# Kernel tuning notes

Hardware: AMD Instinct MI355X
Metric: run time of the kernel (lower is better)

The kernel has to match this reference:

```python
import jax, jax.numpy as jnp
import numpy as np

T = 5
EPS = 1e-05


def setup_inputs() -> dict:
    key = jax.random.key(0)
    X = jax.random.normal(key, (64, 512, 32, 32), dtype=jnp.float32)
    return {"X": X}


def reference(X):
    # IterNorm (training branch): whiten channels via Newton-Schulz inverse sqrt.
    N, C, H, W = X.shape
    x = jnp.transpose(X, (1, 0, 2, 3)).reshape(C, -1)  # [d, m], d=C, m=N*H*W
    d, m = x.shape
    mean = jnp.mean(x, axis=-1, keepdims=True)
    xc = x - mean
    I = jnp.eye(d, dtype=X.dtype)
    # Sigma = eps*I + (1/m) xc xc^T  (addmm(eps, I, 1/m, xc, xc^T))
    Sigma = EPS * I + (xc @ xc.T) / m
    rTr = 1.0 / jnp.trace(Sigma)          # (Sigma * I).sum().reciprocal()
    Sigma_N = Sigma * rTr
    P = I
    for _ in range(T):
        # P_{k+1} = 1.5*P_k - 0.5 * P_k^3 @ Sigma_N
        P = 1.5 * P - 0.5 * (P @ P @ P) @ Sigma_N
    wm = P * jnp.sqrt(rTr)                # whitening matrix ~ Sigma^{-1/2}
    xn = wm @ xc                          # [d, m]
    Xn = jnp.transpose(xn.reshape(C, N, H, W), (1, 0, 2, 3))
    return Xn
```

## Files before the change

kernel.cpp:

```cpp
#include <hip/hip_runtime.h>
#include <math.h>

#define Nn   64
#define Cc   512
#define HWs  1024
#define CHW  (Cc * HWs)
#define Mm   (Nn * HWs)
#define EPSC 1e-5f
#define NBC  128

typedef unsigned int   u32;
typedef unsigned short u16;
typedef __attribute__((ext_vector_type(8))) short  short8;
typedef __attribute__((ext_vector_type(4))) float  floatx4;

__device__ __forceinline__ u16 f2bf(float f) {
    u32 u = __float_as_uint(f);
    u += 0x7fff + ((u >> 16) & 1);
    return (u16)(u >> 16);
}
__device__ __forceinline__ float bf2f(u16 h) {
    return __uint_as_float(((u32)h) << 16);
}

__device__ __forceinline__ void gld_lds16(const u16* g, u16* l) {
    __builtin_amdgcn_global_load_lds(
        (const __attribute__((address_space(1))) u32*)g,
        (__attribute__((address_space(3))) u32*)l, 16, 0, 0);
}

__global__ __launch_bounds__(256) void convert_transpose(const float* __restrict__ X,
                                                         u16* __restrict__ Xbf,
                                                         u16* __restrict__ Xt,
                                                         float* __restrict__ meanP) {
    const int hT = blockIdx.x;
    const int h0 = hT << 6;
    const int c0 = blockIdx.y << 6;
    const int n  = blockIdx.z;
    const int t  = threadIdx.x;
    __shared__ u16   T[64][65];
    __shared__ float red[64][17];

    const float* Xn  = X   + (size_t)n * CHW;
    u16*         Xbn = Xbf + (size_t)n * CHW;
    u16*         Xtn = Xt  + (size_t)n * CHW;

    const int cl = t >> 4;
    const int h4 = (t & 15) << 2;
#pragma unroll
    for (int i = 0; i < 4; ++i) {
        const int c = cl + (i << 4);
        float4 v = *(const float4*)&Xn[(size_t)(c0 + c) * HWs + h0 + h4];
        red[c][t & 15] = v.x + v.y + v.z + v.w;
        u16 b0 = f2bf(v.x), b1 = f2bf(v.y), b2 = f2bf(v.z), b3 = f2bf(v.w);
        *(ushort4*)&Xbn[(size_t)(c0 + c) * HWs + h0 + h4] = make_ushort4(b0, b1, b2, b3);
        T[c][h4]     = b0;
        T[c][h4 + 1] = b1;
        T[c][h4 + 2] = b2;
        T[c][h4 + 3] = b3;
    }
    __syncthreads();
    const int hl = t >> 4;
    const int c4 = (t & 15) << 2;
#pragma unroll
    for (int i = 0; i < 4; ++i) {
        const int h = hl + (i << 4);
        ushort4 pk = make_ushort4(T[c4][h], T[c4 + 1][h], T[c4 + 2][h], T[c4 + 3][h]);
        *(ushort4*)&Xtn[(size_t)(h0 + h) * Cc + c0 + c4] = pk;
    }
    if (t < 64) {
        float s = 0.f;
#pragma unroll
        for (int j = 0; j < 16; ++j) s += red[t][j];
        atomicAdd(&meanP[hT * 512 + c0 + t], s);
    }
}

__global__ __launch_bounds__(256) void gram_mfma(const u16* __restrict__ Xbf,
                                                 float* __restrict__ G) {
    static const int TI[10] = {0,0,0,0,1,1,1,2,2,3};
    static const int TJ[10] = {0,1,2,3,1,2,3,2,3,3};
    const int id = blockIdx.x;
    const int q  = id >> 3;
    const int x  = q % 10;
    const int y  = (id & 7) + ((q / 10) << 3);
    const int i0 = TI[x] << 7;
    const int j0 = TJ[x] << 7;
    const int n0 = y << 1;
    const int t  = threadIdx.x;
    const int w  = t >> 6, l = t & 63;

    __shared__ u16 As[128 * 32];
    __shared__ u16 Bs[128 * 32];

    floatx4 acc[4][4];
#pragma unroll
    for (int mi = 0; mi < 4; ++mi)
#pragma unroll
        for (int ni = 0; ni < 4; ++ni) acc[mi][ni] = (floatx4){0.f, 0.f, 0.f, 0.f};

    const int lr = l >> 2;
    const int lc = (l & 3) << 3;
    const int wm = w >> 1, wn = w & 1;
    const int fm = l & 15, fq = l >> 4;

    for (int n = n0; n < n0 + 2; ++n) {
        const u16* Xn = Xbf + (size_t)n * CHW;
        for (int hw = 0; hw < HWs; hw += 32) {
#pragma unroll
            for (int p = 0; p < 2; ++p) {
                const int g   = w * 2 + p;
                const int row = g * 16 + lr;
                gld_lds16(Xn + (size_t)(i0 + row) * HWs + hw + lc, &As[g * 512]);
                gld_lds16(Xn + (size_t)(j0 + row) * HWs + hw + lc, &Bs[g * 512]);
            }
            __syncthreads();
            short8 a[4], b[4];
#pragma unroll
            for (int mi = 0; mi < 4; ++mi)
                a[mi] = *(const short8*)&As[(wm * 64 + mi * 16 + fm) * 32 + fq * 8];
#pragma unroll
            for (int ni = 0; ni < 4; ++ni)
                b[ni] = *(const short8*)&Bs[(wn * 64 + ni * 16 + fm) * 32 + fq * 8];
#pragma unroll
            for (int mi = 0; mi < 4; ++mi)
#pragma unroll
                for (int ni = 0; ni < 4; ++ni)
                    acc[mi][ni] = __builtin_amdgcn_mfma_f32_16x16x32_bf16(
                        a[mi], b[ni], acc[mi][ni], 0, 0, 0);
            __syncthreads();
        }
    }
#pragma unroll
    for (int mi = 0; mi < 4; ++mi)
#pragma unroll
        for (int ni = 0; ni < 4; ++ni)
#pragma unroll
            for (int r = 0; r < 4; ++r) {
                const int gi = i0 + wm * 64 + mi * 16 + fq * 4 + r;
                const int gj = j0 + wn * 64 + ni * 16 + fm;
                atomicAdd(&G[(size_t)gi * Cc + gj], acc[mi][ni][r]);
            }
}

__device__ __forceinline__ void gridbar(int* bar, int gen) {
    __syncthreads();
    if (threadIdx.x == 0) {
        __threadfence();
        __hip_atomic_fetch_add(bar, 1, __ATOMIC_RELAXED, __HIP_MEMORY_SCOPE_AGENT);
        while (__hip_atomic_load(bar, __ATOMIC_RELAXED, __HIP_MEMORY_SCOPE_AGENT) < gen * NBC)
            __builtin_amdgcn_s_sleep(1);
        __threadfence();
    }
    __syncthreads();
}

__device__ __forceinline__ void mm_panel(const u16* Ah, const u16* Al,
                                         const u16* Bh, const u16* Bl,
                                         int i0, int j0,
                                         float alpha, const float* D, float beta,
                                         float* Cf, u16* Ch, u16* Cl, u16* S) {
    const int t = threadIdx.x, w = t >> 6, l = t & 63;
    const int wm = w >> 1, wn = w & 1, fm = l & 15, fq = l >> 4;
    const u16* src = (w == 0) ? Ah : (w == 1) ? Al : (w == 2) ? Bh : Bl;
    const int rbase = (w < 2) ? i0 : j0;
    const int lr = l >> 2, lc = (l & 3) << 3;

    floatx4 acc[2][2];
#pragma unroll
    for (int mi = 0; mi < 2; ++mi)
#pragma unroll
        for (int ni = 0; ni < 2; ++ni) acc[mi][ni] = (floatx4){0.f, 0.f, 0.f, 0.f};

    auto issue = [&](int cc, int bb) {
        u16* dst = S + bb * 32768 + w * 8192;
        const u16* sp = src + (size_t)rbase * 512 + cc * 128;
#pragma unroll
        for (int s = 0; s < 4; ++s)
#pragma unroll
            for (int g = 0; g < 4; ++g)
                gld_lds16(sp + (size_t)(g * 16 + lr) * 512 + s * 32 + lc,
                          dst + s * 2048 + g * 512);
    };
    auto compute = [&](int bb) {
        const u16* base = S + bb * 32768;
#pragma unroll
        for (int s = 0; s < 4; ++s) {
            short8 ah[2], al[2], bh[2], bl[2];
#pragma unroll
            for (int mi = 0; mi < 2; ++mi) {
                const int ro = s * 2048 + (wm * 32 + mi * 16 + fm) * 32 + fq * 8;
                ah[mi] = *(const short8*)&base[ro];
                al[mi] = *(const short8*)&base[8192 + ro];
            }
#pragma unroll
            for (int ni = 0; ni < 2; ++ni) {
                const int ro = s * 2048 + (wn * 32 + ni * 16 + fm) * 32 + fq * 8;
                bh[ni] = *(const short8*)&base[16384 + ro];
                bl[ni] = *(const short8*)&base[24576 + ro];
            }
#pragma unroll
            for (int mi = 0; mi < 2; ++mi)
#pragma unroll
                for (int ni = 0; ni < 2; ++ni) {
                    acc[mi][ni] = __builtin_amdgcn_mfma_f32_16x16x32_bf16(ah[mi], bh[ni], acc[mi][ni], 0, 0, 0);
                    acc[mi][ni] = __builtin_amdgcn_mfma_f32_16x16x32_bf16(ah[mi], bl[ni], acc[mi][ni], 0, 0, 0);
                    acc[mi][ni] = __builtin_amdgcn_mfma_f32_16x16x32_bf16(al[mi], bh[ni], acc[mi][ni], 0, 0, 0);
                }
        }
    };

    issue(0, 0); issue(1, 1);
    __syncthreads();
    compute(0);
    compute(1);
    __syncthreads();
    issue(2, 0); issue(3, 1);
    __syncthreads();
    compute(0);
    compute(1);

#pragma unroll
    for (int mi = 0; mi < 2; ++mi)
#pragma unroll
        for (int ni = 0; ni < 2; ++ni)
#pragma unroll
            for (int r4 = 0; r4 < 4; ++r4) {
                const int gi = i0 + wm * 32 + mi * 16 + fq * 4 + r4;
                const int gj = j0 + wn * 32 + ni * 16 + fm;
                const size_t idx = (size_t)gi * 512 + gj;
                float v = alpha * acc[mi][ni][r4];
                if (D) v += beta * D[idx];
                if (Cf) Cf[idx] = v;
                const u16 h = f2bf(v);
                Ch[idx] = h;
                Cl[idx] = f2bf(v - bf2f(h));
            }
}

__global__ __launch_bounds__(256) void ns_chain(
    const float* G, const float* meanP, float* scal, int* bar, float* wmmv,
    u16* Sh, u16* Sl, u16* PhA, u16* PlA, u16* PhB, u16* PlB,
    u16* T2h, u16* T2l, u16* Wh, u16* Wl, float* PfA, float* PfB) {
    __shared__ u16   S[65536];
    __shared__ float meanL[512];
    __shared__ float redL[4];
    const int t = threadIdx.x, b = blockIdx.x;
    const int w = t >> 6, l = t & 63;

    float tp = 0.f;
#pragma unroll
    for (int cb = 0; cb < 2; ++cb) {
        const int c = t + (cb << 8);
        float s = 0.f;
#pragma unroll
        for (int q = 0; q < 16; ++q) s += meanP[(q << 9) + c];
        const float mc = s * (1.0f / Mm);
        meanL[c] = mc;
        tp += G[(size_t)c * 513] * (1.0f / Mm) - mc * mc;
    }
#pragma unroll
    for (int o = 32; o > 0; o >>= 1) tp += __shfl_xor(tp, o);
    if (l == 0) redL[w] = tp;
    __syncthreads();
    const float tr  = redL[0] + redL[1] + redL[2] + redL[3] + (float)Cc * EPSC;
    const float rtr = 1.0f / tr;
    const float sr  = sqrtf(rtr);
    if (b == 0 && t == 0) { scal[0] = rtr; scal[1] = sr; }

#pragma unroll
    for (int k2 = 0; k2 < 8; ++k2) {
        const int e = (b << 11) + (k2 << 8) + t;
        const int i = e >> 9, j = e & 511;
        const float g = (i <= j) ? G[((size_t)i << 9) + j] : G[((size_t)j << 9) + i];
        float sig = g * (1.0f / Mm) - meanL[i] * meanL[j];
        if (i == j) sig += EPSC;
        const float sN = sig * rtr;
        const u16 sh = f2bf(sN);
        Sh[e] = sh;
        Sl[e] = f2bf(sN - bf2f(sh));
        const float p1 = ((i == j) ? 1.5f : 0.f) - 0.5f * sN;
        PfA[e] = p1;
        const u16 ph = f2bf(p1);
        PhA[e] = ph;
        PlA[e] = f2bf(p1 - bf2f(ph));
    }
    int gen = 0;
    gridbar(bar, ++gen);

    u16 *ph = PhA, *pl = PlA, *qh = PhB, *ql = PlB;
    float *pf = PfA, *qf = PfB;
    const int i0 = ((b & 63) >> 3) << 6, j0 = (b & 7) << 6;
    for (int it = 0; it < 4; ++it) {
        if (b < 64)
            mm_panel(ph, pl, ph, pl, i0, j0, 1.f, nullptr, 0.f,
                     nullptr, T2h, T2l, S);
        else
            mm_panel(ph, pl, Sh, Sl, i0, j0, 1.f, nullptr, 0.f,
                     nullptr, Wh, Wl, S);
        gridbar(bar, ++gen);
        if (b < 64)
            mm_panel(T2h, T2l, Wh, Wl, i0, j0, -0.5f, pf, 1.5f,
                     qf, qh, ql, S);
        gridbar(bar, ++gen);
        { u16* x = ph; ph = qh; qh = x; }
        { u16* x = pl; pl = ql; ql = x; }
        { float* x = pf; pf = qf; qf = x; }
    }

    {
        const int c = (b << 2) + (t >> 6);
        float s = 0.f;
#pragma unroll
        for (int jj = 0; jj < 8; ++jj) {
            const int j = l + (jj << 6);
            s += pf[((size_t)c << 9) + j] * meanL[j];
        }
#pragma unroll
        for (int o = 32; o > 0; o >>= 1) s += __shfl_xor(s, o);
        if (l == 0) wmmv[c] = s * sr;
    }
}

__global__ __launch_bounds__(256) void whiten_mfma(const u16* __restrict__ Xt,
                                                   const u16* __restrict__ Pbf,
                                                   const float* __restrict__ wmm,
                                                   const float* __restrict__ scal,
                                                   float* __restrict__ out) {
    const int id  = blockIdx.x;
    const int m   = (id >> 3) & 3;
    const int grp = (id & 7) + ((id >> 5) << 3);
    const int c0  = m << 7;
    const int h0  = (grp & 7) << 7;
    const int n   = grp >> 3;
    const int t   = threadIdx.x;
    const int w   = t >> 6, l = t & 63;

    __shared__ char smem[128 * 68 * 4];
    u16* As = (u16*)smem;
    u16* Bs = As + 4096;
    float* Ep = (float*)smem;

    floatx4 acc[4][4];
#pragma unroll
    for (int mi = 0; mi < 4; ++mi)
#pragma unroll
        for (int ni = 0; ni < 4; ++ni) acc[mi][ni] = (floatx4){0.f, 0.f, 0.f, 0.f};

    const int lr = l >> 2;
    const int lc = (l & 3) << 3;
    const int wm = w >> 1, wn = w & 1;
    const int fm = l & 15, fq = l >> 4;

    const u16* Xn = Xt + (size_t)n * CHW;

    for (int kk = 0; kk < Cc; kk += 32) {
#pragma unroll
        for (int p = 0; p < 2; ++p) {
            const int g   = w * 2 + p;
            const int row = g * 16 + lr;
            gld_lds16(Xn  + (size_t)(h0 + row) * Cc + kk + lc, &As[g * 512]);
            gld_lds16(Pbf + (size_t)(c0 + row) * Cc + kk + lc, &Bs[g * 512]);
        }
        __syncthreads();
        short8 a[4], b[4];
#pragma unroll
        for (int mi = 0; mi < 4; ++mi)
            a[mi] = *(const short8*)&As[(wm * 64 + mi * 16 + fm) * 32 + fq * 8];
#pragma unroll
        for (int ni = 0; ni < 4; ++ni)
            b[ni] = *(const short8*)&Bs[(wn * 64 + ni * 16 + fm) * 32 + fq * 8];
#pragma unroll
        for (int mi = 0; mi < 4; ++mi)
#pragma unroll
            for (int ni = 0; ni < 4; ++ni)
                acc[mi][ni] = __builtin_amdgcn_mfma_f32_16x16x32_bf16(
                    a[mi], b[ni], acc[mi][ni], 0, 0, 0);
        __syncthreads();
    }

    const float sr = scal[1];
    float wv[4];
#pragma unroll
    for (int ni = 0; ni < 4; ++ni) wv[ni] = wmm[c0 + wn * 64 + ni * 16 + fm];
    float* outn = out + (size_t)n * CHW;

#pragma unroll
    for (int mp = 0; mp < 2; ++mp) {
        __syncthreads();
#pragma unroll
        for (int p = 0; p < 2; ++p) {
            const int mi = mp * 2 + p;
#pragma unroll
            for (int ni = 0; ni < 4; ++ni) {
                const int row  = wn * 64 + ni * 16 + fm;
                const int slot = wm * 32 + p * 16 + fq * 4;
                floatx4 v = acc[mi][ni] * sr - wv[ni];
                *(floatx4*)&Ep[row * 68 + slot] = v;
            }
        }
        __syncthreads();
#pragma unroll
        for (int jj = 0; jj < 8; ++jj) {
            const int idx = jj * 256 + t;
            const int row = idx >> 4;
            const int s4  = (idx & 15) << 2;
            const int wmr = s4 >> 5;
            const int within = s4 & 31;
            float4 v = *(const float4*)&Ep[row * 68 + s4];
            *(float4*)&outn[(size_t)(c0 + row) * HWs + h0 + wmr * 64 + mp * 32 + within] = v;
        }
    }
}

__global__ __launch_bounds__(256) void mean_kernel(const float* __restrict__ X,
                                                   float* __restrict__ mean) {
    const int c = blockIdx.x;
    const int t = threadIdx.x;
    float s = 0.f;
    for (int n = 0; n < Nn; ++n) {
        const float4* p = (const float4*)(X + (size_t)n * CHW + (size_t)c * HWs);
        float4 v = p[t];
        s += v.x + v.y + v.z + v.w;
    }
    __shared__ float red[256];
    red[t] = s;
    __syncthreads();
    for (int o = 128; o > 0; o >>= 1) {
        if (t < o) red[t] += red[t + o];
        __syncthreads();
    }
    if (t == 0) mean[c] = red[0] * (1.0f / Mm);
}

__global__ __launch_bounds__(256) void trace_fb(const float* __restrict__ G,
                                                const float* __restrict__ mean,
                                                float* __restrict__ scal) {
    const int t = threadIdx.x;
    float s = 0.f;
    for (int i = t; i < Cc; i += 256)
        s += G[(size_t)i * Cc + i] * (1.0f / Mm) - mean[i] * mean[i];
    __shared__ float red[256];
    red[t] = s;
    __syncthreads();
    for (int o = 128; o > 0; o >>= 1) {
        if (t < o) red[t] += red[t + o];
        __syncthreads();
    }
    if (t == 0) {
        const float tr  = red[0] + (float)Cc * EPSC;
        const float rtr = 1.0f / tr;
        scal[0] = rtr;
        scal[1] = sqrtf(rtr);
    }
}

__global__ __launch_bounds__(256) void gram_kernel(const float* __restrict__ X,
                                                   float* __restrict__ G) {
    const int ti = blockIdx.x >> 3, tj = blockIdx.x & 7;
    const int i0 = ti << 6, j0 = tj << 6;
    const int n0 = blockIdx.y << 3;
    const int t  = threadIdx.x;
    const int tx = t & 15, ty = t >> 4;
    __shared__ float As[64][33];
    __shared__ float Bs[64][33];
    float acc[4][4] = {};
    const int lc = t & 31;
    const int lr0 = t >> 5;
    for (int n = n0; n < n0 + 8; ++n) {
        const float* Xn = X + (size_t)n * CHW;
        for (int hw0 = 0; hw0 < HWs; hw0 += 32) {
#pragma unroll
            for (int r = 0; r < 8; ++r) {
                const int row = lr0 + (r << 3);
                As[row][lc] = Xn[(size_t)(i0 + row) * HWs + hw0 + lc];
                Bs[row][lc] = Xn[(size_t)(j0 + row) * HWs + hw0 + lc];
            }
            __syncthreads();
#pragma unroll
            for (int k = 0; k < 32; ++k) {
                float a[4], b[4];
#pragma unroll
                for (int r = 0; r < 4; ++r) a[r] = As[(ty << 2) + r][k];
#pragma unroll
                for (int cn = 0; cn < 4; ++cn) b[cn] = Bs[(tx << 2) + cn][k];
#pragma unroll
                for (int r = 0; r < 4; ++r)
#pragma unroll
                    for (int cn = 0; cn < 4; ++cn) acc[r][cn] += a[r] * b[cn];
            }
            __syncthreads();
        }
    }
#pragma unroll
    for (int r = 0; r < 4; ++r)
#pragma unroll
        for (int cn = 0; cn < 4; ++cn)
            atomicAdd(&G[(size_t)(i0 + (ty << 2) + r) * Cc + j0 + (tx << 2) + cn],
                      acc[r][cn]);
}

__global__ __launch_bounds__(256) void sigman_full_kernel(const float* __restrict__ G,
                                                          const float* __restrict__ mean,
                                                          const float* __restrict__ scal,
                                                          float* __restrict__ S,
                                                          float* __restrict__ P) {
    const int e = blockIdx.x * 256 + threadIdx.x;
    const int i = e >> 9, j = e & 511;
    const float rtr = scal[0];
    float sig = G[e] * (1.0f / Mm) - mean[i] * mean[j];
    if (i == j) sig += EPSC;
    S[e] = sig * rtr;
    P[e] = (i == j) ? 1.f : 0.f;
}

__global__ __launch_bounds__(256) void mm512_kernel(const float* __restrict__ A,
                                                    const float* __restrict__ B,
                                                    float* __restrict__ C,
                                                    float alpha,
                                                    const float* __restrict__ D,
                                                    float beta) {
    const int ti = blockIdx.x >> 3, tj = blockIdx.x & 7;
    const int i0 = ti << 6, j0 = tj << 6;
    const int t  = threadIdx.x;
    const int tx = t & 15, ty = t >> 4;
    __shared__ float As[64][33];
    __shared__ float Bs[32][65];
    float acc[4][4] = {};
    const int lcA = t & 31, lrA = t >> 5;
    const int lcB = t & 63, lrB = t >> 6;
    for (int k0 = 0; k0 < 512; k0 += 32) {
#pragma unroll
        for (int r = 0; r < 8; ++r) {
            const int row = lrA + (r << 3);
            As[row][lcA] = A[(size_t)(i0 + row) * 512 + k0 + lcA];
        }
#pragma unroll
        for (int r = 0; r < 8; ++r) {
            const int row = lrB + (r << 2);
            Bs[row][lcB] = B[(size_t)(k0 + row) * 512 + j0 + lcB];
        }
        __syncthreads();
#pragma unroll
        for (int k = 0; k < 32; ++k) {
            float a[4], b[4];
#pragma unroll
            for (int r = 0; r < 4; ++r) a[r] = As[(ty << 2) + r][k];
#pragma unroll
            for (int cn = 0; cn < 4; ++cn) b[cn] = Bs[k][(tx << 2) + cn];
#pragma unroll
            for (int r = 0; r < 4; ++r)
#pragma unroll
                for (int cn = 0; cn < 4; ++cn) acc[r][cn] += a[r] * b[cn];
        }
        __syncthreads();
    }
#pragma unroll
    for (int r = 0; r < 4; ++r) {
        const size_t idx = (size_t)(i0 + (ty << 2) + r) * 512 + j0 + (tx << 2);
        float4 v;
        v.x = alpha * acc[r][0];
        v.y = alpha * acc[r][1];
        v.z = alpha * acc[r][2];
        v.w = alpha * acc[r][3];
        if (D) {
            const float4 d = *(const float4*)(D + idx);
            v.x += beta * d.x; v.y += beta * d.y; v.z += beta * d.z; v.w += beta * d.w;
        }
        *(float4*)(C + idx) = v;
    }
}

__global__ __launch_bounds__(128) void wmm_kernel(const float* __restrict__ P,
                                                  const float* __restrict__ mean,
                                                  const float* __restrict__ scal,
                                                  float* __restrict__ wmm) {
    const int c = blockIdx.x, t = threadIdx.x;
    float s = 0.f;
    for (int j = t; j < Cc; j += 128) s += P[(size_t)c * Cc + j] * mean[j];
    __shared__ float red[128];
    red[t] = s;
    __syncthreads();
    for (int o = 64; o > 0; o >>= 1) {
        if (t < o) red[t] += red[t + o];
        __syncthreads();
    }
    if (t == 0) wmm[c] = red[0] * scal[1];
}

__global__ __launch_bounds__(256) void whiten_kernel(const float* __restrict__ X,
                                                     const float* __restrict__ P,
                                                     const float* __restrict__ wmm,
                                                     const float* __restrict__ scal,
                                                     float* __restrict__ out) {
    const int c0 = blockIdx.x << 6;
    const int h0 = blockIdx.y << 6;
    const int n  = blockIdx.z;
    const int t  = threadIdx.x;
    const int tx = t & 15, ty = t >> 4;
    __shared__ float Ps[64][33];
    __shared__ float Xs[32][65];
    float acc[4][4] = {};
    const int lcA = t & 31, lrA = t >> 5;
    const int lcB = t & 63, lrB = t >> 6;
    const float* Xn = X + (size_t)n * CHW;
    for (int k0 = 0; k0 < 512; k0 += 32) {
#pragma unroll
        for (int r = 0; r < 8; ++r) {
            const int row = lrA + (r << 3);
            Ps[row][lcA] = P[(size_t)(c0 + row) * 512 + k0 + lcA];
        }
#pragma unroll
        for (int r = 0; r < 8; ++r) {
            const int row = lrB + (r << 2);
            Xs[row][lcB] = Xn[(size_t)(k0 + row) * HWs + h0 + lcB];
        }
        __syncthreads();
#pragma unroll
        for (int k = 0; k < 32; ++k) {
            float a[4], b[4];
#pragma unroll
            for (int r = 0; r < 4; ++r) a[r] = Ps[(ty << 2) + r][k];
#pragma unroll
            for (int cn = 0; cn < 4; ++cn) b[cn] = Xs[k][(tx << 2) + cn];
#pragma unroll
            for (int r = 0; r < 4; ++r)
#pragma unroll
                for (int cn = 0; cn < 4; ++cn) acc[r][cn] += a[r] * b[cn];
        }
        __syncthreads();
    }
    const float sr = scal[1];
#pragma unroll
    for (int r = 0; r < 4; ++r) {
        const int c = c0 + (ty << 2) + r;
        const float wv = wmm[c];
        float4 v;
        v.x = sr * acc[r][0] - wv;
        v.y = sr * acc[r][1] - wv;
        v.z = sr * acc[r][2] - wv;
        v.w = sr * acc[r][3] - wv;
        *(float4*)(out + (size_t)n * CHW + (size_t)c * HWs + h0 + (tx << 2)) = v;
    }
}

extern "C" void kernel_launch(void* const* d_in, const int* in_sizes, int n_in,
                              void* d_out, int out_size, void* d_ws, size_t ws_size,
                              hipStream_t stream) {
    const float* X = (const float*)d_in[0];
    float* out     = (float*)d_out;

    const size_t NU16 = 33554432;
    const size_t NM   = 262144;
    const size_t NEED = NU16 * 2 * 2
                      + NM * 10 * 2
                      + (NM + 8192 + 32 + 512 + 512 + 2 * NM) * 4;

    if (ws_size >= NEED) {
        u16* Xbf = (u16*)d_ws;
        u16* Xt  = Xbf + NU16;
        u16* Sh  = Xt  + NU16;
        u16* Sl  = Sh + NM;
        u16* PhA = Sl + NM;
        u16* PlA = PhA + NM;
        u16* PhB = PlA + NM;
        u16* PlB = PhB + NM;
        u16* T2h = PlB + NM;
        u16* T2l = T2h + NM;
        u16* Wh  = T2l + NM;
        u16* Wl  = Wh + NM;
        float* G     = (float*)(Wl + NM);
        float* meanP = G + NM;
        float* scal  = meanP + 8192;
        int*   bar   = (int*)(scal + 16);
        float* mean  = (float*)(bar + 16);
        float* wmm   = mean + 512;
        float* PfA   = wmm + 512;
        float* PfB   = PfA + NM;

        hipMemsetAsync(G, 0, (NM + 8192 + 32) * sizeof(float), stream);
        convert_transpose<<<dim3(16, 8, 64), 256, 0, stream>>>(X, Xbf, Xt, meanP);
        gram_mfma<<<320, 256, 0, stream>>>(Xbf, G);
        ns_chain<<<NBC, 256, 0, stream>>>(G, meanP, scal, bar, wmm,
                                          Sh, Sl, PhA, PlA, PhB, PlB,
                                          T2h, T2l, Wh, Wl, PfA, PfB);
        whiten_mfma<<<2048, 256, 0, stream>>>(Xt, PhA, wmm, scal, out);
    } else {
        float* ws   = (float*)d_ws;
        float* mean = ws;
        float* wmm  = ws + 512;
        float* scal = ws + 1024;
        float* G    = ws + 2048;
        float* S    = G + 262144;
        float* Pa   = S + 262144;
        float* Pb   = Pa + 262144;
        float* P2   = Pb + 262144;
        float* P3   = P2 + 262144;

        mean_kernel<<<512, 256, 0, stream>>>(X, mean);
        hipMemsetAsync(G, 0, sizeof(float) * 262144, stream);
        gram_kernel<<<dim3(64, 8), 256, 0, stream>>>(X, G);
        trace_fb<<<1, 256, 0, stream>>>(G, mean, scal);
        sigman_full_kernel<<<1024, 256, 0, stream>>>(G, mean, scal, S, Pa);

        float* P  = Pa;
        float* Pn = Pb;
        for (int it = 0; it < 5; ++it) {
            mm512_kernel<<<64, 256, 0, stream>>>(P, P, P2, 1.f, nullptr, 0.f);
            mm512_kernel<<<64, 256, 0, stream>>>(P2, P, P3, 1.f, nullptr, 0.f);
            mm512_kernel<<<64, 256, 0, stream>>>(P3, S, Pn, -0.5f, P, 1.5f);
            float* tmp = P; P = Pn; Pn = tmp;
        }

        wmm_kernel<<<512, 128, 0, stream>>>(P, mean, scal, wmm);
        whiten_kernel<<<dim3(8, 16, 64), 256, 0, stream>>>(X, P, wmm, scal, out);
    }
}
```

Measured before the change: 512.5 us.

## Double-buffer LDS in gram, NS chain and whiten GEMMs; widen gram grid

Adds ping-pong LDS buffers to the gram, whiten and Newton-Schulz panel GEMMs so the next K-slice global-to-LDS load overlaps the current MFMA work. The gram kernel now gives each block one sample instead of two and launches twice as many blocks. The NS chain panel kernel moves from K=128 chunks to K=64 chunks in an 8-step pipelined loop, which halves its LDS footprint. It also uses half-height 32-row tiles so all 128 blocks take part in the second GEMM of each iteration instead of only 64. In exchange there are twice as many atomics into G from the gram kernel and more barriers per tile.

Result: slower. 524.0 us (+2.2%).

```diff
diff --git a/kernel.cpp b/kernel.cpp
--- a/kernel.cpp
+++ b/kernel.cpp
@@ -86,12 +86,12 @@
     const int y  = (id & 7) + ((q / 10) << 3);
     const int i0 = TI[x] << 7;
     const int j0 = TJ[x] << 7;
-    const int n0 = y << 1;
+    const int n  = y;
     const int t  = threadIdx.x;
     const int w  = t >> 6, l = t & 63;
 
-    __shared__ u16 As[128 * 32];
-    __shared__ u16 Bs[128 * 32];
+    __shared__ u16 As[2][4096];
+    __shared__ u16 Bs[2][4096];
 
     floatx4 acc[4][4];
 #pragma unroll
@@ -104,32 +104,37 @@
     const int wm = w >> 1, wn = w & 1;
     const int fm = l & 15, fq = l >> 4;
 
-    for (int n = n0; n < n0 + 2; ++n) {
-        const u16* Xn = Xbf + (size_t)n * CHW;
-        for (int hw = 0; hw < HWs; hw += 32) {
-#pragma unroll
-            for (int p = 0; p < 2; ++p) {
-                const int g   = w * 2 + p;
-                const int row = g * 16 + lr;
-                gld_lds16(Xn + (size_t)(i0 + row) * HWs + hw + lc, &As[g * 512]);
-                gld_lds16(Xn + (size_t)(j0 + row) * HWs + hw + lc, &Bs[g * 512]);
-            }
-            __syncthreads();
-            short8 a[4], b[4];
-#pragma unroll
-            for (int mi = 0; mi < 4; ++mi)
-                a[mi] = *(const short8*)&As[(wm * 64 + mi * 16 + fm) * 32 + fq * 8];
+    const u16* Xn = Xbf + (size_t)n * CHW;
+
+    auto issue = [&](int k, int bb) {
+#pragma unroll
+        for (int p = 0; p < 2; ++p) {
+            const int g   = w * 2 + p;
+            const int row = g * 16 + lr;
+            gld_lds16(Xn + (size_t)(i0 + row) * HWs + (k << 5) + lc, &As[bb][g * 512]);
+            gld_lds16(Xn + (size_t)(j0 + row) * HWs + (k << 5) + lc, &Bs[bb][g * 512]);
+        }
+    };
+
+    issue(0, 0);
+    __syncthreads();
+    for (int k = 0; k < 32; ++k) {
+        if (k < 31) issue(k + 1, (k + 1) & 1);
+        const int bb = k & 1;
+        short8 a[4], b[4];
+#pragma unroll
+        for (int mi = 0; mi < 4; ++mi)
+            a[mi] = *(const short8*)&As[bb][(wm * 64 + mi * 16 + fm) * 32 + fq * 8];
+#pragma unroll
+        for (int ni = 0; ni < 4; ++ni)
+            b[ni] = *(const short8*)&Bs[bb][(wn * 64 + ni * 16 + fm) * 32 + fq * 8];
+#pragma unroll
+        for (int mi = 0; mi < 4; ++mi)
 #pragma unroll
             for (int ni = 0; ni < 4; ++ni)
-                b[ni] = *(const short8*)&Bs[(wn * 64 + ni * 16 + fm) * 32 + fq * 8];
-#pragma unroll
-            for (int mi = 0; mi < 4; ++mi)
-#pragma unroll
-                for (int ni = 0; ni < 4; ++ni)
-                    acc[mi][ni] = __builtin_amdgcn_mfma_f32_16x16x32_bf16(
-                        a[mi], b[ni], acc[mi][ni], 0, 0, 0);
-            __syncthreads();
-        }
+                acc[mi][ni] = __builtin_amdgcn_mfma_f32_16x16x32_bf16(
+                    a[mi], b[ni], acc[mi][ni], 0, 0, 0);
+        __syncthreads();
     }
 #pragma unroll
     for (int mi = 0; mi < 4; ++mi)
@@ -155,52 +160,63 @@
     __syncthreads();
 }
 
-__device__ __forceinline__ void mm_panel(const u16* Ah, const u16* Al,
-                                         const u16* Bh, const u16* Bl,
-                                         int i0, int j0,
-                                         float alpha, const float* D, float beta,
-                                         float* Cf, u16* Ch, u16* Cl, u16* S) {
+template <int MR>
+__device__ __forceinline__ void mm_bk64(const u16* Ah, const u16* Al,
+                                        const u16* Bh, const u16* Bl,
+                                        int i0, int j0,
+                                        float alpha, const float* D, float beta,
+                                        float* Cf, u16* Ch, u16* Cl, u16* S) {
     const int t = threadIdx.x, w = t >> 6, l = t & 63;
     const int wm = w >> 1, wn = w & 1, fm = l & 15, fq = l >> 4;
-    const u16* src = (w == 0) ? Ah : (w == 1) ? Al : (w == 2) ? Bh : Bl;
+    const int lr = l >> 2, lc = (l & 3) << 3;
+    constexpr int MI     = MR / 32;
+    constexpr int OFF_AL = MR * 64;
+    constexpr int OFF_BH = 2 * MR * 64;
+    constexpr int OFF_BL = 2 * MR * 64 + 4096;
+    constexpr int BUFSZ  = 2 * MR * 64 + 8192;
+
+    const u16* src  = (w == 0) ? Ah : (w == 1) ? Al : (w == 2) ? Bh : Bl;
     const int rbase = (w < 2) ? i0 : j0;
-    const int lr = l >> 2, lc = (l & 3) << 3;
-
-    floatx4 acc[2][2];
-#pragma unroll
-    for (int mi = 0; mi < 2; ++mi)
+    const int R     = (w < 2) ? MR : 64;
+    const int OFF   = (w == 0) ? 0 : (w == 1) ? OFF_AL : (w == 2) ? OFF_BH : OFF_BL;
+
+    floatx4 acc[MI][2];
+#pragma unroll
+    for (int mi = 0; mi < MI; ++mi)
 #pragma unroll
         for (int ni = 0; ni < 2; ++ni) acc[mi][ni] = (floatx4){0.f, 0.f, 0.f, 0.f};
 
-    auto issue = [&](int cc, int bb) {
-        u16* dst = S + bb * 32768 + w * 8192;
-        const u16* sp = src + (size_t)rbase * 512 + cc * 128;
-#pragma unroll
-        for (int s = 0; s < 4; ++s)
-#pragma unroll
-            for (int g = 0; g < 4; ++g)
+    auto issue = [&](int c, int bb) {
+        u16* dst = S + bb * BUFSZ + OFF;
+        const u16* sp = src + (size_t)rbase * 512 + (c << 6);
+#pragma unroll
+        for (int s = 0; s < 2; ++s)
+#pragma unroll 4
+            for (int g = 0; g < (R >> 4); ++g)
                 gld_lds16(sp + (size_t)(g * 16 + lr) * 512 + s * 32 + lc,
-                          dst + s * 2048 + g * 512);
+                          dst + s * R * 32 + g * 512);
     };
     auto compute = [&](int bb) {
-        const u16* base = S + bb * 32768;
-#pragma unroll
-        for (int s = 0; s < 4; ++s) {
-            short8 ah[2], al[2], bh[2], bl[2];
-#pragma unroll
-            for (int mi = 0; mi < 2; ++mi) {
-                const int ro = s * 2048 + (wm * 32 + mi * 16 + fm) * 32 + fq * 8;
-                ah[mi] = *(const short8*)&base[ro];
-                al[mi] = *(const short8*)&base[8192 + ro];
+        const u16* base = S + bb * BUFSZ;
+#pragma unroll
+        for (int s = 0; s < 2; ++s) {
+            short8 ah[MI], al[MI], bh[2], bl[2];
+#pragma unroll
+            for (int mi = 0; mi < MI; ++mi) {
+                const int r = wm * (MR / 2) + mi * 16 + fm;
+                const int o = s * MR * 32 + r * 32 + fq * 8;
+                ah[mi] = *(const short8*)&base[o];
+                al[mi] = *(const short8*)&base[OFF_AL + o];
             }
 #pragma unroll
             for (int ni = 0; ni < 2; ++ni) {
-                const int ro = s * 2048 + (wn * 32 + ni * 16 + fm) * 32 + fq * 8;
-                bh[ni] = *(const short8*)&base[16384 + ro];
-                bl[ni] = *(const short8*)&base[24576 + ro];
+                const int r = wn * 32 + ni * 16 + fm;
+                const int o = s * 2048 + r * 32 + fq * 8;
+                bh[ni] = *(const short8*)&base[OFF_BH + o];
+                bl[ni] = *(const short8*)&base[OFF_BL + o];
             }
 #pragma unroll
-            for (int mi = 0; mi < 2; ++mi)
+            for (int mi = 0; mi < MI; ++mi)
 #pragma unroll
                 for (int ni = 0; ni < 2; ++ni) {
                     acc[mi][ni] = __builtin_amdgcn_mfma_f32_16x16x32_bf16(ah[mi], bh[ni], acc[mi][ni], 0, 0, 0);
@@ -210,23 +226,21 @@
         }
     };
 
-    issue(0, 0); issue(1, 1);
-    __syncthreads();
-    compute(0);
-    compute(1);
-    __syncthreads();
-    issue(2, 0); issue(3, 1);
-    __syncthreads();
-    compute(0);
-    compute(1);
-
-#pragma unroll
-    for (int mi = 0; mi < 2; ++mi)
+    issue(0, 0);
+    __syncthreads();
+    for (int c = 0; c < 8; ++c) {
+        if (c < 7) issue(c + 1, (c + 1) & 1);
+        compute(c & 1);
+        __syncthreads();
+    }
+
+#pragma unroll
+    for (int mi = 0; mi < MI; ++mi)
 #pragma unroll
         for (int ni = 0; ni < 2; ++ni)
 #pragma unroll
             for (int r4 = 0; r4 < 4; ++r4) {
-                const int gi = i0 + wm * 32 + mi * 16 + fq * 4 + r4;
+                const int gi = i0 + wm * (MR / 2) + mi * 16 + fq * 4 + r4;
                 const int gj = j0 + wn * 32 + ni * 16 + fm;
                 const size_t idx = (size_t)gi * 512 + gj;
                 float v = alpha * acc[mi][ni][r4];
@@ -242,7 +256,7 @@
     const float* G, const float* meanP, float* scal, int* bar, float* wmmv,
     u16* Sh, u16* Sl, u16* PhA, u16* PlA, u16* PhB, u16* PlB,
     u16* T2h, u16* T2l, u16* Wh, u16* Wl, float* PfA, float* PfB) {
-    __shared__ u16   S[65536];
+    __shared__ u16   S[32768];
     __shared__ float meanL[512];
     __shared__ float redL[4];
     const int t = threadIdx.x, b = blockIdx.x;
@@ -290,18 +304,18 @@
 
     u16 *ph = PhA, *pl = PlA, *qh = PhB, *ql = PlB;
     float *pf = PfA, *qf = PfB;
-    const int i0 = ((b & 63) >> 3) << 6, j0 = (b & 7) << 6;
+    const int i0a = ((b & 63) >> 3) << 6, j0a = (b & 7) << 6;
+    const int i0b = (b >> 3) << 5,        j0b = (b & 7) << 6;
     for (int it = 0; it < 4; ++it) {
         if (b < 64)
-            mm_panel(ph, pl, ph, pl, i0, j0, 1.f, nullptr, 0.f,
-                     nullptr, T2h, T2l, S);
+            mm_bk64<64>(ph, pl, ph, pl, i0a, j0a, 1.f, nullptr, 0.f,
+                        nullptr, T2h, T2l, S);
         else
-            mm_panel(ph, pl, Sh, Sl, i0, j0, 1.f, nullptr, 0.f,
-                     nullptr, Wh, Wl, S);
+            mm_bk64<64>(ph, pl, Sh, Sl, i0a, j0a, 1.f, nullptr, 0.f,
+                        nullptr, Wh, Wl, S);
         gridbar(bar, ++gen);
-        if (b < 64)
-            mm_panel(T2h, T2l, Wh, Wl, i0, j0, -0.5f, pf, 1.5f,
-                     qf, qh, ql, S);
+        mm_bk64<32>(T2h, T2l, Wh, Wl, i0b, j0b, -0.5f, pf, 1.5f,
+                    qf, qh, ql, S);
         gridbar(bar, ++gen);
         { u16* x = ph; ph = qh; qh = x; }
         { u16* x = pl; pl = ql; ql = x; }
@@ -337,8 +351,8 @@
     const int w   = t >> 6, l = t & 63;
 
     __shared__ char smem[128 * 68 * 4];
-    u16* As = (u16*)smem;
-    u16* Bs = As + 4096;
+    u16* AsB = (u16*)smem;
+    u16* BsB = AsB + 8192;
     float* Ep = (float*)smem;
 
     floatx4 acc[4][4];
@@ -354,22 +368,28 @@
 
     const u16* Xn = Xt + (size_t)n * CHW;
 
-    for (int kk = 0; kk < Cc; kk += 32) {
+    auto issue = [&](int k, int bb) {
 #pragma unroll
         for (int p = 0; p < 2; ++p) {
             const int g   = w * 2 + p;
             const int row = g * 16 + lr;
-            gld_lds16(Xn  + (size_t)(h0 + row) * Cc + kk + lc, &As[g * 512]);
-            gld_lds16(Pbf + (size_t)(c0 + row) * Cc + kk + lc, &Bs[g * 512]);
-        }
-        __syncthreads();
+            gld_lds16(Xn  + (size_t)(h0 + row) * Cc + (k << 5) + lc, &AsB[bb * 4096 + g * 512]);
+            gld_lds16(Pbf + (size_t)(c0 + row) * Cc + (k << 5) + lc, &BsB[bb * 4096 + g * 512]);
+        }
+    };
+
+    issue(0, 0);
+    __syncthreads();
+    for (int k = 0; k < 16; ++k) {
+        if (k < 15) issue(k + 1, (k + 1) & 1);
+        const int bb = k & 1;
         short8 a[4], b[4];
 #pragma unroll
         for (int mi = 0; mi < 4; ++mi)
-            a[mi] = *(const short8*)&As[(wm * 64 + mi * 16 + fm) * 32 + fq * 8];
+            a[mi] = *(const short8*)&AsB[bb * 4096 + (wm * 64 + mi * 16 + fm) * 32 + fq * 8];
 #pragma unroll
         for (int ni = 0; ni < 4; ++ni)
-            b[ni] = *(const short8*)&Bs[(wn * 64 + ni * 16 + fm) * 32 + fq * 8];
+            b[ni] = *(const short8*)&BsB[bb * 4096 + (wn * 64 + ni * 16 + fm) * 32 + fq * 8];
 #pragma unroll
         for (int mi = 0; mi < 4; ++mi)
 #pragma unroll
@@ -680,7 +700,7 @@
 
         hipMemsetAsync(G, 0, (NM + 8192 + 32) * sizeof(float), stream);
         convert_transpose<<<dim3(16, 8, 64), 256, 0, stream>>>(X, Xbf, Xt, meanP);
-        gram_mfma<<<320, 256, 0, stream>>>(Xbf, G);
+        gram_mfma<<<640, 256, 0, stream>>>(Xbf, G);
         ns_chain<<<NBC, 256, 0, stream>>>(G, meanP, scal, bar, wmm,
                                           Sh, Sl, PhA, PlA, PhB, PlB,
                                           T2h, T2l, Wh, Wl, PfA, PfB);
```
